# Kernel tuning notes

Measured on AMD Instinct MI355X. Metric: run time of the kernel, lower is better.

The kernel has to match this reference:

```python
import jax, jax.numpy as jnp
import numpy as np

N_NODES = 100000
N_EDGES = 320000
N_GRAPHS = 4096
HID = 256
NUM_FEAT = 28


def setup_inputs() -> dict:
    key = jax.random.key(0)
    ks = jax.random.split(key, 20)
    inp = {}
    inp['x'] = jax.random.normal(ks[0], (N_NODES, NUM_FEAT), dtype=jnp.float32)
    inp['edge_index'] = jax.random.randint(ks[1], (2, N_EDGES), 0, N_NODES, dtype=jnp.int64)
    inp['batch'] = jnp.sort(jax.random.randint(ks[2], (N_NODES,), 0, N_GRAPHS, dtype=jnp.int64))
    def lin(k, out_d, in_d, scale=None):
        s = scale if scale is not None else 1.0 / np.sqrt(in_d)
        return jax.random.uniform(k, (out_d, in_d), jnp.float32, -s, s)
    # GraphConv layer l: W_rel (neighbor aggregate), b_rel, W_root (self)
    dims = [(HID, NUM_FEAT), (HID, HID), (HID, HID), (HID, HID)]
    for i, (o, d) in enumerate(dims, 1):
        inp[f'W{i}_rel'] = lin(ks[2 + 3 * i], o, d)
        inp[f'b{i}_rel'] = jnp.zeros((o,), jnp.float32)
        inp[f'W{i}_root'] = lin(ks[3 + 3 * i], o, d)
    inp['fc1_w'] = lin(ks[15], HID, 4 * HID)
    inp['fc1_b'] = jnp.zeros((HID,), jnp.float32)
    inp['fc2_w'] = lin(ks[16], HID, HID)
    inp['fc2_b'] = jnp.zeros((HID,), jnp.float32)
    inp['fc3_w'] = lin(ks[17], HID, HID)
    inp['fc3_b'] = jnp.zeros((HID,), jnp.float32)
    inp['fc4_w'] = lin(ks[18], 1, HID)
    inp['fc4_b'] = jnp.zeros((1,), jnp.float32)
    return inp


def _graph_conv(x, src, dst, W_rel, b_rel, W_root):
    # PyG GraphConv (aggr='add'): out = lin_rel(sum_{j->i} x_j) + lin_root(x_i)
    agg = jax.ops.segment_sum(x[src], dst, num_segments=N_NODES)  # [N, d]
    return agg @ W_rel.T + b_rel + x @ W_root.T


def reference(x, edge_index, batch,
              W1_rel, b1_rel, W1_root, W2_rel, b2_rel, W2_root,
              W3_rel, b3_rel, W3_root, W4_rel, b4_rel, W4_root,
              fc1_w, fc1_b, fc2_w, fc2_b, fc3_w, fc3_b, fc4_w, fc4_b):
    src, dst = edge_index[0], edge_index[1]
    x1 = jax.nn.relu(_graph_conv(x, src, dst, W1_rel, b1_rel, W1_root))
    x2 = jax.nn.relu(_graph_conv(x1, src, dst, W2_rel, b2_rel, W2_root))
    x3 = jax.nn.relu(_graph_conv(x2, src, dst, W3_rel, b3_rel, W3_root))
    x4 = jax.nn.relu(_graph_conv(x3, src, dst, W4_rel, b4_rel, W4_root))
    h = jnp.concatenate([x1, x2, x3, x4], axis=-1)  # [N, 4*HID]
    # global mean pool over graphs
    sums = jax.ops.segment_sum(h, batch, num_segments=N_GRAPHS)  # [G, 4*HID]
    cnts = jax.ops.segment_sum(jnp.ones((h.shape[0],), h.dtype), batch, num_segments=N_GRAPHS)
    g = sums / jnp.maximum(cnts, 1.0)[:, None]
    g = jax.nn.relu(g @ fc1_w.T + fc1_b)
    g = jax.nn.relu(g @ fc2_w.T + fc2_b)
    g = jax.nn.relu(g @ fc3_w.T + fc3_b)
    out = g @ fc4_w.T + fc4_b  # [G, 1]
    return out.reshape(-1)
```

## Files before the change

### kernel.cpp

```cpp
#include <hip/hip_runtime.h>
#include <hip/hip_bf16.h>
#include <cstdio>

#define HID 256

using short8  = __attribute__((ext_vector_type(8))) short;
using floatx4 = __attribute__((ext_vector_type(4))) float;

typedef const unsigned int __attribute__((address_space(1)))* as1_cuintp;
typedef unsigned int __attribute__((address_space(3)))* as3_uintp;

__device__ inline unsigned short bf16_rn(float x) {
    unsigned u = __float_as_uint(x);
    return (unsigned short)((u + 0x7FFFu + ((u >> 16) & 1u)) >> 16);
}
__device__ inline float bf2f(unsigned short u) {
    return __uint_as_float(((unsigned)u) << 16);
}

__global__ void marker_k(float* __restrict__ out, int n, float v) {
    int i = blockIdx.x * blockDim.x + threadIdx.x;
    if (i < n) out[i] = v;
}

__global__ void detect64_k(const unsigned* __restrict__ eiw, int E,
                           const unsigned* __restrict__ bw, int Nh,
                           int* __restrict__ any_nonzero) {
    int total = E + Nh;
    unsigned loc = 0;
    for (int i = blockIdx.x * blockDim.x + threadIdx.x; i < total;
         i += gridDim.x * blockDim.x) {
        loc |= (i < E) ? eiw[2 * i + 1] : bw[2 * (i - E) + 1];
    }
    if (loc) atomicOr(any_nonzero, 1);
}

__global__ void norm_idx_k(const int* __restrict__ src, int* __restrict__ dst,
                           int n, const int* __restrict__ any_nonzero) {
    int is64 = (any_nonzero[0] == 0);
    for (int i = blockIdx.x * blockDim.x + threadIdx.x; i < n;
         i += gridDim.x * blockDim.x) {
        dst[i] = is64 ? src[2 * i] : src[i];
    }
}

__global__ void pool_bounds_k(const int* __restrict__ batch, int N, int G,
                              int* __restrict__ starts) {
    int g = blockIdx.x * blockDim.x + threadIdx.x;
    if (g > G) return;
    int lo = 0, hi = N;
    while (lo < hi) {
        int mid = (lo + hi) >> 1;
        if (batch[mid] < g) lo = mid + 1; else hi = mid;
    }
    starts[g] = lo;
}

__global__ void deg_count_k(const int* __restrict__ ei, int E, int N,
                            int* __restrict__ deg) {
    int e = blockIdx.x * blockDim.x + threadIdx.x;
    if (e >= E) return;
    int s = ei[e];
    int d = ei[E + e];
    if ((unsigned)s >= (unsigned)N || (unsigned)d >= (unsigned)N) return;
    atomicAdd(&deg[d], 1);
}

#define SCAN_BLK 256

__global__ __launch_bounds__(SCAN_BLK) void scan_a_k(const int* __restrict__ deg,
                                                     int* __restrict__ bsum, int N) {
    __shared__ int red[SCAN_BLK];
    int i = blockIdx.x * SCAN_BLK + threadIdx.x;
    int v = (i < N) ? deg[i] : 0;
    red[threadIdx.x] = v;
    __syncthreads();
#pragma unroll
    for (int off = SCAN_BLK / 2; off > 0; off >>= 1) {
        if (threadIdx.x < off) red[threadIdx.x] += red[threadIdx.x + off];
        __syncthreads();
    }
    if (threadIdx.x == 0) bsum[blockIdx.x] = red[0];
}

__global__ __launch_bounds__(1024) void scan_b_k(int* __restrict__ bsum, int nb) {
    __shared__ int tsum[1024];
    int t = threadIdx.x;
    int v = (t < nb) ? bsum[t] : 0;
    tsum[t] = v;
    __syncthreads();
    for (int off = 1; off < 1024; off <<= 1) {
        int u = (t >= off) ? tsum[t - off] : 0;
        __syncthreads();
        tsum[t] += u;
        __syncthreads();
    }
    if (t < nb) bsum[t] = tsum[t] - v;
}

__global__ __launch_bounds__(SCAN_BLK) void scan_c_k(const int* __restrict__ deg,
                                                     const int* __restrict__ bsum,
                                                     int* __restrict__ row_ptr, int N) {
    __shared__ int tsum[SCAN_BLK];
    int t = threadIdx.x;
    int i = blockIdx.x * SCAN_BLK + t;
    int v = (i < N) ? deg[i] : 0;
    tsum[t] = v;
    __syncthreads();
    for (int off = 1; off < SCAN_BLK; off <<= 1) {
        int u = (t >= off) ? tsum[t - off] : 0;
        __syncthreads();
        tsum[t] += u;
        __syncthreads();
    }
    if (i <= N) row_ptr[i] = tsum[t] - v + bsum[blockIdx.x];
}

__global__ __launch_bounds__(1024) void scan_rowptr_k(const int* __restrict__ deg,
                                                      int* __restrict__ row_ptr, int N) {
    __shared__ int tsum[1024];
    int t = threadIdx.x;
    int chunk = (N + 1023) / 1024;
    int lo = t * chunk;
    int hi = min(lo + chunk, N);
    int s = 0;
    for (int i = lo; i < hi; i++) s += deg[i];
    tsum[t] = s;
    __syncthreads();
    for (int off = 1; off < 1024; off <<= 1) {
        int v = (t >= off) ? tsum[t - off] : 0;
        __syncthreads();
        tsum[t] += v;
        __syncthreads();
    }
    int run = (t == 0) ? 0 : tsum[t - 1];
    for (int i = lo; i < hi; i++) { row_ptr[i] = run; run += deg[i]; }
    if (hi >= N && lo <= N) row_ptr[N] = run;
}

__global__ void fill_csr_k(const int* __restrict__ ei, int E, int N,
                           const int* __restrict__ row_ptr, int* __restrict__ cursor,
                           int* __restrict__ esrc) {
    int e = blockIdx.x * blockDim.x + threadIdx.x;
    if (e >= E) return;
    int s = ei[e];
    int d = ei[E + e];
    if ((unsigned)s >= (unsigned)N || (unsigned)d >= (unsigned)N) return;
    int pos = atomicAdd(&cursor[d], 1);
    esrc[row_ptr[d] + pos] = s;
}

__global__ void gather28_k(const float* __restrict__ x, const int* __restrict__ row_ptr,
                           const int* __restrict__ esrc, float* __restrict__ Q28, int N) {
    int gid = blockIdx.x * blockDim.x + threadIdx.x;
    int node = gid >> 5;
    if (node >= N) return;
    int lane = gid & 31;
    if (lane >= 28) return;
    int s = row_ptr[node], e = row_ptr[node + 1];
    float acc = 0.f;
    for (int i = s; i < e; i++) {
        int src = esrc[i];
        acc += x[(size_t)src * 28 + lane];
    }
    Q28[(size_t)node * 28 + lane] = acc;
}

__global__ void gather256_k(const float* __restrict__ P, const int* __restrict__ row_ptr,
                            const int* __restrict__ esrc, float* __restrict__ Q, int N) {
    int gid = blockIdx.x * blockDim.x + threadIdx.x;
    int node = gid >> 6;
    if (node >= N) return;
    int lane = gid & 63;
    int s = row_ptr[node], e = row_ptr[node + 1];
    float4 acc = make_float4(0.f, 0.f, 0.f, 0.f);
    for (int i = s; i < e; i++) {
        int src = esrc[i];
        float4 v = *(const float4*)(P + (size_t)src * HID + lane * 4);
        acc.x += v.x; acc.y += v.y; acc.z += v.z; acc.w += v.w;
    }
    *(float4*)(Q + (size_t)node * HID + lane * 4) = acc;
}

__global__ __launch_bounds__(256) void l1_fused_k(
    const float* __restrict__ x, const float* __restrict__ agg,
    const float* __restrict__ Wrel, const float* __restrict__ Wroot,
    const float* __restrict__ bias, float* __restrict__ out, int M) {
    __shared__ float As[64][28];
    __shared__ float Xs[64][28];
    int t = threadIdx.x;
    int n0 = blockIdx.x * 64;
    float wrel[28], wroot[28];
#pragma unroll
    for (int k = 0; k < 28; k++) {
        wrel[k]  = Wrel[t * 28 + k];
        wroot[k] = Wroot[t * 28 + k];
    }
    float b = bias[t];
    for (int idx = t; idx < 64 * 28; idx += 256) {
        int r = idx / 28;
        int c = idx - r * 28;
        int gr = n0 + r;
        As[r][c] = (gr < M) ? agg[(size_t)gr * 28 + c] : 0.f;
        Xs[r][c] = (gr < M) ? x[(size_t)gr * 28 + c] : 0.f;
    }
    __syncthreads();
    int nmax = min(64, M - n0);
    for (int n = 0; n < nmax; n++) {
        float acc = b;
#pragma unroll
        for (int k4 = 0; k4 < 28; k4 += 4) {
            float4 a  = *(const float4*)&As[n][k4];
            float4 xx = *(const float4*)&Xs[n][k4];
            acc += a.x * wrel[k4] + a.y * wrel[k4 + 1] + a.z * wrel[k4 + 2] + a.w * wrel[k4 + 3];
            acc += xx.x * wroot[k4] + xx.y * wroot[k4 + 1] + xx.z * wroot[k4 + 2] + xx.w * wroot[k4 + 3];
        }
        out[(size_t)(n0 + n) * HID + t] = fmaxf(acc, 0.f);
    }
}

__global__ void wsplit6_k(const float* W0, const float* W1, const float* W2,
                          const float* W3, const float* W4, const float* W5,
                          unsigned short* __restrict__ out_hl, int n) {
    int i = blockIdx.x * blockDim.x + threadIdx.x;
    if (i >= n) return;
    const float* W = (blockIdx.y == 0) ? W0 : (blockIdx.y == 1) ? W1 :
                     (blockIdx.y == 2) ? W2 : (blockIdx.y == 3) ? W3 :
                     (blockIdx.y == 4) ? W4 : W5;
    unsigned short* o = out_hl + (size_t)blockIdx.y * 131072;
    float a = W[i];
    unsigned short h = bf16_rn(a);
    unsigned short lo = bf16_rn(a - bf2f(h));
    int col = i >> 8;
    int k   = i & 255;
    int ch  = k >> 5;
    int sg  = (k >> 3) & 3;
    int e   = k & 7;
    int gp  = sg ^ ((col >> 1) & 3);
    size_t base = (size_t)ch * 16384 + (size_t)col * 32 + gp * 8 + e;
    o[base] = h;
    o[base + 8192] = lo;
}

#define LSTR 40

__global__ __launch_bounds__(256) void gemm_strip_mfma_k(
    const float* __restrict__ Q, const unsigned short* __restrict__ Wr_hl,
    float* __restrict__ P, const unsigned short* __restrict__ Wo_hl,
    const float* __restrict__ bias, int M) {
    __shared__ unsigned short Ah[64 * LSTR], Al[64 * LSTR];
    __shared__ unsigned short Wlin[16384];
    int t = threadIdx.x;
    int brow = blockIdx.x * 64;
    int w = t >> 6;
    int l = t & 63;

    floatx4 acc[4][4];
#pragma unroll
    for (int i = 0; i < 4; i++)
#pragma unroll
        for (int j = 0; j < 4; j++) acc[i][j] = (floatx4){0.f, 0.f, 0.f, 0.f};

    int srow = t >> 2;
    int sg   = t & 3;

    for (int ch = 0; ch < 16; ch++) {
        int phase2 = (ch >= 8);
        const float* A = phase2 ? P : Q;
        const unsigned short* Whl = phase2 ? Wo_hl : Wr_hl;
        int kbase = (ch & 7) * 32;

        {
            int gr = brow + srow;
            float v[8];
            if (gr < M) {
                float4 u0 = *(const float4*)(A + (size_t)gr * HID + kbase + sg * 8);
                float4 u1 = *(const float4*)(A + (size_t)gr * HID + kbase + sg * 8 + 4);
                v[0] = u0.x; v[1] = u0.y; v[2] = u0.z; v[3] = u0.w;
                v[4] = u1.x; v[5] = u1.y; v[6] = u1.z; v[7] = u1.w;
            } else {
#pragma unroll
                for (int j = 0; j < 8; j++) v[j] = 0.f;
            }
            union { unsigned short us[8]; short8 v8; } hh, ll;
#pragma unroll
            for (int j = 0; j < 8; j++) {
                unsigned short h = bf16_rn(v[j]);
                float hf = __uint_as_float(((unsigned)h) << 16);
                hh.us[j] = h;
                ll.us[j] = bf16_rn(v[j] - hf);
            }
            int base = srow * LSTR + sg * 8;
            *(short8*)(Ah + base) = hh.v8;
            *(short8*)(Al + base) = ll.v8;
        }
        {
            const char* wg = (const char*)(Whl + (size_t)(ch & 7) * 16384);
#pragma unroll
            for (int i = 0; i < 8; i++) {
                int boff = w * 8192 + i * 1024;
                __builtin_amdgcn_global_load_lds(
                    (as1_cuintp)(const void*)(wg + boff + l * 16),
                    (as3_uintp)(void*)((char*)Wlin + boff),
                    16, 0, 0);
            }
        }
        __syncthreads();

        int frow = l & 15;
        int fg   = l >> 4;
        short8 ahf[4], alf[4], whf[4], wlf[4];
#pragma unroll
        for (int rt = 0; rt < 4; rt++) {
            int base = (rt * 16 + frow) * LSTR + fg * 8;
            ahf[rt] = *(short8*)(Ah + base);
            alf[rt] = *(short8*)(Al + base);
        }
#pragma unroll
        for (int ct = 0; ct < 4; ct++) {
            int col = w * 64 + ct * 16 + frow;
            int gp = fg ^ ((col >> 1) & 3);
            int base = col * 32 + gp * 8;
            whf[ct] = *(short8*)(Wlin + base);
            wlf[ct] = *(short8*)(Wlin + 8192 + base);
        }
#pragma unroll
        for (int rt = 0; rt < 4; rt++)
#pragma unroll
            for (int ct = 0; ct < 4; ct++) {
                acc[rt][ct] = __builtin_amdgcn_mfma_f32_16x16x32_bf16(
                    ahf[rt], whf[ct], acc[rt][ct], 0, 0, 0);
                acc[rt][ct] = __builtin_amdgcn_mfma_f32_16x16x32_bf16(
                    alf[rt], whf[ct], acc[rt][ct], 0, 0, 0);
                acc[rt][ct] = __builtin_amdgcn_mfma_f32_16x16x32_bf16(
                    ahf[rt], wlf[ct], acc[rt][ct], 0, 0, 0);
            }
        __syncthreads();
    }

#pragma unroll
    for (int ct = 0; ct < 4; ct++) {
        int gc = w * 64 + ct * 16 + (l & 15);
        float bs = bias[gc];
#pragma unroll
        for (int rt = 0; rt < 4; rt++) {
            floatx4 a = acc[rt][ct];
#pragma unroll
            for (int r = 0; r < 4; r++) {
                int gr = brow + rt * 16 + (l >> 4) * 4 + r;
                if (gr < M)
                    P[(size_t)gr * HID + gc] = fmaxf(a[r] + bs, 0.f);
            }
        }
    }
}

__global__ __launch_bounds__(256) void pool_slice_k(const float* __restrict__ xl,
                                                    const int* __restrict__ starts,
                                                    float* __restrict__ gslice, int N) {
    int g = blockIdx.x;
    int t = threadIdx.x;
    int s = starts[g], e = starts[g + 1];
    s = max(0, min(s, N));
    e = max(s, min(e, N));
    float a = 0.f;
    for (int n = s; n < e; n++) a += xl[(size_t)n * HID + t];
    float inv = 1.f / (float)max(e - s, 1);
    gslice[(size_t)g * 1024 + t] = a * inv;
}

#define BM 64
#define BN 64
#define BK 32
#define LP 68

__global__ __launch_bounds__(256) void gemm_dual_k(
    const float* __restrict__ A1, int lda1, const float* __restrict__ W1,
    const float* __restrict__ A2, int lda2, const float* __restrict__ W2,
    const float* __restrict__ bias, float* __restrict__ out, int ldout,
    int M, int K1, int K2, int relu) {
    __shared__ float As[BK][LP];
    __shared__ float Ws[BK][LP];
    int t = threadIdx.x;
    int brow = blockIdx.x * BM;
    int bcol = blockIdx.y * BN;
    int tx = t & 15, ty = t >> 4;
    float acc[4][4] = {{0.f}};
    int Ktot = K1 + K2;
    int srow = t >> 3;
    int sk4 = (t & 7) << 2;

    for (int kk = 0; kk < Ktot; kk += BK) {
        int phase2 = (kk >= K1);
        const float* A = phase2 ? A2 : A1;
        const float* W = phase2 ? W2 : W1;
        int lda = phase2 ? lda2 : lda1;
        int ldw = phase2 ? K2 : K1;
        int kbase = phase2 ? (kk - K1) : kk;
#pragma unroll
        for (int i = 0; i < 2; i++) {
            int r = srow + i * 32;
            int gr = brow + r;
            float4 v = make_float4(0.f, 0.f, 0.f, 0.f);
            if (gr < M) v = *(const float4*)(A + (size_t)gr * lda + kbase + sk4);
            As[sk4 + 0][r] = v.x; As[sk4 + 1][r] = v.y;
            As[sk4 + 2][r] = v.z; As[sk4 + 3][r] = v.w;
            float4 w = *(const float4*)(W + (size_t)(bcol + r) * ldw + kbase + sk4);
            Ws[sk4 + 0][r] = w.x; Ws[sk4 + 1][r] = w.y;
            Ws[sk4 + 2][r] = w.z; Ws[sk4 + 3][r] = w.w;
        }
        __syncthreads();
#pragma unroll
        for (int k = 0; k < BK; k++) {
            float4 a = *(const float4*)&As[k][ty << 2];
            float4 w = *(const float4*)&Ws[k][tx << 2];
            float av[4] = {a.x, a.y, a.z, a.w};
            float wv[4] = {w.x, w.y, w.z, w.w};
#pragma unroll
            for (int i = 0; i < 4; i++)
#pragma unroll
                for (int j = 0; j < 4; j++)
                    acc[i][j] = fmaf(av[i], wv[j], acc[i][j]);
        }
        __syncthreads();
    }
#pragma unroll
    for (int i = 0; i < 4; i++) {
        int gr = brow + (ty << 2) + i;
        if (gr >= M) continue;
#pragma unroll
        for (int j = 0; j < 4; j++) {
            int gc = bcol + (tx << 2) + j;
            float v = acc[i][j] + bias[gc];
            if (relu) v = fmaxf(v, 0.f);
            out[(size_t)gr * ldout + gc] = v;
        }
    }
}

__global__ void fc4_k(const float* __restrict__ in, const float* __restrict__ w,
                      const float* __restrict__ b, float* __restrict__ out, int M) {
    int gid = blockIdx.x * blockDim.x + threadIdx.x;
    int row = gid >> 6;
    if (row >= M) return;
    int lane = gid & 63;
    float4 v  = *(const float4*)(in + (size_t)row * HID + lane * 4);
    float4 ww = *(const float4*)(w + lane * 4);
    float acc = v.x * ww.x + v.y * ww.y + v.z * ww.z + v.w * ww.w;
#pragma unroll
    for (int off = 32; off; off >>= 1) acc += __shfl_down(acc, off);
    if (lane == 0) out[row] = acc + b[0];
}

extern "C" void kernel_launch(void* const* d_in, const int* in_sizes, int n_in,
                              void* d_out, int out_size, void* d_ws, size_t ws_size,
                              hipStream_t stream) {
    const int N = in_sizes[0] / 28;
    const int E = in_sizes[1] / 2;
    const int G = out_size;

    const float* x        = (const float*)d_in[0];
    const int*   ei_raw   = (const int*)d_in[1];
    const int*   b_raw    = (const int*)d_in[2];
    const float* W1_rel  = (const float*)d_in[3];
    const float* b1      = (const float*)d_in[4];
    const float* W1_root = (const float*)d_in[5];
    const float* W2_rel  = (const float*)d_in[6];
    const float* b2      = (const float*)d_in[7];
    const float* W2_root = (const float*)d_in[8];
    const float* W3_rel  = (const float*)d_in[9];
    const float* b3      = (const float*)d_in[10];
    const float* W3_root = (const float*)d_in[11];
    const float* W4_rel  = (const float*)d_in[12];
    const float* b4      = (const float*)d_in[13];
    const float* W4_root = (const float*)d_in[14];
    const float* fc1_w = (const float*)d_in[15];
    const float* fc1_b = (const float*)d_in[16];
    const float* fc2_w = (const float*)d_in[17];
    const float* fc2_b = (const float*)d_in[18];
    const float* fc3_w = (const float*)d_in[19];
    const float* fc3_b = (const float*)d_in[20];
    const float* fc4_w = (const float*)d_in[21];
    const float* fc4_b = (const float*)d_in[22];
    float* out = (float*)d_out;

    size_t fN  = (size_t)N * HID;
    size_t off_P      = 0;
    size_t off_Q      = off_P + fN;
    size_t off_gpool  = off_Q + fN;
    size_t off_t1     = off_gpool + (size_t)G * 1024;
    size_t off_t2     = off_t1 + (size_t)G * HID;
    size_t off_ei     = off_t2 + (size_t)G * HID;
    size_t off_batch  = off_ei + (size_t)2 * E;
    size_t off_starts = off_batch + (size_t)N;
    size_t off_flag   = off_starts + (size_t)(G + 1);
    size_t off_deg    = off_flag + 1;
    size_t off_cur    = off_deg + (size_t)N;
    size_t off_rowp   = off_cur + (size_t)N;
    size_t off_bsum   = off_rowp + (size_t)(N + 1);
    size_t off_esrc   = off_bsum + 1024;
    size_t off_wsplit = (off_esrc + (size_t)E + 3) & ~(size_t)3;
    size_t need = (off_wsplit + 393216 + 16) * 4;

    if (ws_size < need) {
        fprintf(stderr, "[kernel_launch] ws too small: ws=%zu need=%zu\n", ws_size, need);
        marker_k<<<(G + 255) / 256, 256, 0, stream>>>(out, G, (float)(ws_size >> 20));
        return;
    }

    float* wsf   = (float*)d_ws;
    float* P     = wsf + off_P;
    float* Q     = wsf + off_Q;
    float* gpool = wsf + off_gpool;
    float* t1    = wsf + off_t1;
    float* t2    = wsf + off_t2;
    int* nei     = (int*)(wsf + off_ei);
    int* nbatch  = (int*)(wsf + off_batch);
    int* starts  = (int*)(wsf + off_starts);
    int* flag    = (int*)(wsf + off_flag);
    int* deg     = (int*)(wsf + off_deg);
    int* cursor  = (int*)(wsf + off_cur);
    int* row_ptr = (int*)(wsf + off_rowp);
    int* bsum    = (int*)(wsf + off_bsum);
    int* esrc    = (int*)(wsf + off_esrc);
    unsigned short* wsplit = (unsigned short*)(wsf + off_wsplit);

    hipMemsetAsync(flag, 0, sizeof(int), stream);
    detect64_k<<<1024, 256, 0, stream>>>((const unsigned*)ei_raw, E,
                                         (const unsigned*)b_raw, N / 2, flag);
    norm_idx_k<<<1024, 256, 0, stream>>>(ei_raw, nei, 2 * E, flag);
    norm_idx_k<<<512, 256, 0, stream>>>(b_raw, nbatch, N, flag);

    pool_bounds_k<<<(G + 1 + 255) / 256, 256, 0, stream>>>(nbatch, N, G, starts);

    hipMemsetAsync(deg, 0, 2 * (size_t)N * sizeof(int), stream);
    deg_count_k<<<(E + 255) / 256, 256, 0, stream>>>(nei, E, N, deg);
    int nb = (N + 1 + SCAN_BLK - 1) / SCAN_BLK;
    if (nb <= 1024) {
        scan_a_k<<<nb, SCAN_BLK, 0, stream>>>(deg, bsum, N);
        scan_b_k<<<1, 1024, 0, stream>>>(bsum, nb);
        scan_c_k<<<nb, SCAN_BLK, 0, stream>>>(deg, bsum, row_ptr, N);
    } else {
        scan_rowptr_k<<<1, 1024, 0, stream>>>(deg, row_ptr, N);
    }
    fill_csr_k<<<(E + 255) / 256, 256, 0, stream>>>(nei, E, N, row_ptr, cursor, esrc);

    wsplit6_k<<<dim3((65536 + 255) / 256, 6), 256, 0, stream>>>(
        W2_rel, W2_root, W3_rel, W3_root, W4_rel, W4_root, wsplit, 65536);

    int nstrips = (N + 63) / 64;

    gather28_k<<<((size_t)N * 32 + 255) / 256, 256, 0, stream>>>(x, row_ptr, esrc, Q, N);
    l1_fused_k<<<nstrips, 256, 0, stream>>>(x, Q, W1_rel, W1_root, b1, P, N);
    pool_slice_k<<<G, 256, 0, stream>>>(P, starts, gpool + 0, N);

    const float* bb[3] = {b2, b3, b4};
    for (int l = 0; l < 3; l++) {
        gather256_k<<<((size_t)N * 64 + 255) / 256, 256, 0, stream>>>(P, row_ptr, esrc, Q, N);
        gemm_strip_mfma_k<<<nstrips, 256, 0, stream>>>(
            Q, wsplit + (size_t)(2 * l) * 131072,
            P, wsplit + (size_t)(2 * l + 1) * 131072, bb[l], N);
        pool_slice_k<<<G, 256, 0, stream>>>(P, starts, gpool + 256 * (l + 1), N);
    }

    dim3 gdimG(G / BM, HID / BN);
    gemm_dual_k<<<gdimG, 256, 0, stream>>>(gpool, 1024, fc1_w, nullptr, 0, nullptr,
                                           fc1_b, t1, HID, G, 1024, 0, 1);
    gemm_dual_k<<<gdimG, 256, 0, stream>>>(t1, HID, fc2_w, nullptr, 0, nullptr,
                                           fc2_b, t2, HID, G, HID, 0, 1);
    gemm_dual_k<<<gdimG, 256, 0, stream>>>(t2, HID, fc3_w, nullptr, 0, nullptr,
                                           fc3_b, t1, HID, G, HID, 0, 1);
    fc4_k<<<(G * 64 + 255) / 256, 256, 0, stream>>>(t1, fc4_w, fc4_b, out, G);
}
```

Baseline: 984.4 us.

## Halve weight LDS buffer and stream low-part weights during MFMA

The GEMM strip kernel now keeps only the high bf16 half of each weight chunk in LDS. It loads the low half into the same buffer asynchronously while the high-weight MFMAs run, then reloads fragments and does the remaining MFMAs. The weight LDS issue is also moved ahead of the A conversion. This halves weight LDS usage, which may raise occupancy, and overlaps the second weight load with compute. In exchange it adds explicit waitcnt and sched barriers, a serialising vmcnt wait, and a second fragment read each chunk.

```diff
diff --git a/kernel.cpp b/kernel.cpp
--- a/kernel.cpp
+++ b/kernel.cpp
@@ -248,8 +248,9 @@
     const float* __restrict__ Q, const unsigned short* __restrict__ Wr_hl,
     float* __restrict__ P, const unsigned short* __restrict__ Wo_hl,
     const float* __restrict__ bias, int M) {
-    __shared__ unsigned short Ah[64 * LSTR], Al[64 * LSTR];
-    __shared__ unsigned short Wlin[16384];
+    __shared__ __attribute__((aligned(16))) unsigned short Ah[64 * LSTR];
+    __shared__ __attribute__((aligned(16))) unsigned short Al[64 * LSTR];
+    __shared__ __attribute__((aligned(16))) unsigned short Wbuf[8192];
     int t = threadIdx.x;
     int brow = blockIdx.x * 64;
     int w = t >> 6;
@@ -270,6 +271,17 @@
         const unsigned short* Whl = phase2 ? Wo_hl : Wr_hl;
         int kbase = (ch & 7) * 32;
 
+        {
+            const char* wg = (const char*)(Whl + (size_t)(ch & 7) * 16384) + w * 4096;
+            char* ld = (char*)Wbuf + w * 4096;
+#pragma unroll
+            for (int i = 0; i < 4; i++) {
+                __builtin_amdgcn_global_load_lds(
+                    (as1_cuintp)(const void*)(wg + i * 1024 + l * 16),
+                    (as3_uintp)(void*)(ld + i * 1024),
+                    16, 0, 0);
+            }
+        }
         {
             int gr = brow + srow;
             float v[8];
@@ -294,22 +306,11 @@
             *(short8*)(Ah + base) = hh.v8;
             *(short8*)(Al + base) = ll.v8;
         }
-        {
-            const char* wg = (const char*)(Whl + (size_t)(ch & 7) * 16384);
-#pragma unroll
-            for (int i = 0; i < 8; i++) {
-                int boff = w * 8192 + i * 1024;
-                __builtin_amdgcn_global_load_lds(
-                    (as1_cuintp)(const void*)(wg + boff + l * 16),
-                    (as3_uintp)(void*)((char*)Wlin + boff),
-                    16, 0, 0);
-            }
-        }
         __syncthreads();
 
         int frow = l & 15;
         int fg   = l >> 4;
-        short8 ahf[4], alf[4], whf[4], wlf[4];
+        short8 ahf[4], alf[4], wf[4];
 #pragma unroll
         for (int rt = 0; rt < 4; rt++) {
             int base = (rt * 16 + frow) * LSTR + fg * 8;
@@ -320,21 +321,44 @@
         for (int ct = 0; ct < 4; ct++) {
             int col = w * 64 + ct * 16 + frow;
             int gp = fg ^ ((col >> 1) & 3);
-            int base = col * 32 + gp * 8;
-            whf[ct] = *(short8*)(Wlin + base);
-            wlf[ct] = *(short8*)(Wlin + 8192 + base);
+            wf[ct] = *(short8*)(Wbuf + col * 32 + gp * 8);
+        }
+        asm volatile("s_waitcnt lgkmcnt(0)" ::: "memory");
+        __builtin_amdgcn_sched_barrier(0);
+        {
+            const char* wg = (const char*)(Whl + (size_t)(ch & 7) * 16384 + 8192) + w * 4096;
+            char* ld = (char*)Wbuf + w * 4096;
+#pragma unroll
+            for (int i = 0; i < 4; i++) {
+                __builtin_amdgcn_global_load_lds(
+                    (as1_cuintp)(const void*)(wg + i * 1024 + l * 16),
+                    (as3_uintp)(void*)(ld + i * 1024),
+                    16, 0, 0);
+            }
         }
 #pragma unroll
         for (int rt = 0; rt < 4; rt++)
 #pragma unroll
             for (int ct = 0; ct < 4; ct++) {
                 acc[rt][ct] = __builtin_amdgcn_mfma_f32_16x16x32_bf16(
-                    ahf[rt], whf[ct], acc[rt][ct], 0, 0, 0);
+                    ahf[rt], wf[ct], acc[rt][ct], 0, 0, 0);
                 acc[rt][ct] = __builtin_amdgcn_mfma_f32_16x16x32_bf16(
-                    alf[rt], whf[ct], acc[rt][ct], 0, 0, 0);
+                    alf[rt], wf[ct], acc[rt][ct], 0, 0, 0);
+            }
+        asm volatile("s_waitcnt vmcnt(0)" ::: "memory");
+        __builtin_amdgcn_sched_barrier(0);
+#pragma unroll
+        for (int ct = 0; ct < 4; ct++) {
+            int col = w * 64 + ct * 16 + frow;
+            int gp = fg ^ ((col >> 1) & 3);
+            wf[ct] = *(short8*)(Wbuf + col * 32 + gp * 8);
+        }
+#pragma unroll
+        for (int rt = 0; rt < 4; rt++)
+#pragma unroll
+            for (int ct = 0; ct < 4; ct++)
                 acc[rt][ct] = __builtin_amdgcn_mfma_f32_16x16x32_bf16(
-                    ahf[rt], wlf[ct], acc[rt][ct], 0, 0, 0);
-            }
+                    ahf[rt], wf[ct], acc[rt][ct], 0, 0, 0);
         __syncthreads();
     }
 
```

Result: no change. 970.9 us, median of 2 (-1.4%).
